# Optimization experiments

Measured on AMD Instinct MI355X. Metric: run time of the kernel, lower is better.

The kernel has to match this reference:

```python
import jax, jax.numpy as jnp
import numpy as np

T, B, L, D = 4, 16, 1024, 256
TAU = 2.0        # LIF membrane time constant
V_TH = 1.0       # spike threshold
ALPHA = 4.0      # sigmoid surrogate slope (spikingjelly default)


@jax.custom_vjp
def spike(x):
    # Heaviside step with sigmoid surrogate gradient
    return (x >= 0.0).astype(x.dtype)

def _spike_fwd(x):
    return spike(x), x

def _spike_bwd(x, g):
    s = jax.nn.sigmoid(ALPHA * x)
    return (g * ALPHA * s * (1.0 - s),)

spike.defvjp(_spike_fwd, _spike_bwd)


def lif_multistep(x):
    """MultiStepLIFNode(tau=2, hard reset to 0, detach_reset=True) over dim 0.
    x: [T, B, 1, D] -> spikes [T, B, 1, D]."""
    def step(v, xt):
        h = v + (xt - v) / TAU                 # neuronal charge
        s = spike(h - V_TH)                    # fire
        v_next = h * (1.0 - jax.lax.stop_gradient(s))  # detached hard reset
        return v_next, s
    _, spikes = jax.lax.scan(step, jnp.zeros_like(x[0]), x)
    return spikes


def setup_inputs() -> dict:
    key = jax.random.key(0)
    kq, kk, kv, km = jax.random.split(key, 4)
    q = jax.random.normal(kq, (T, B, L, D), jnp.float32)
    k = jax.random.normal(kk, (T, B, L, D), jnp.float32)
    v = jax.random.normal(kv, (T, B, L, D), jnp.float32)
    mask = jax.random.randint(km, (T, B, L), 0, 2) > 0  # bool padding mask
    return {"q": q, "k": k, "v": v, "mask": mask}


def reference(q, k, v, mask):
    # mode='s' path of ScaledDotProductAttention
    attn = k * v                                      # [T,B,L,D]
    attn = jnp.where(mask[..., None], 0.0, attn)      # masked_fill(mask, 0)
    kv = jnp.sum(attn, axis=-2, keepdims=True)        # [T,B,1,D]
    kv = lif_multistep(kv)                            # spiking gate over T
    output = q * kv                                   # broadcast over L
    return output, attn
```

## Files before the change

kernel.cpp:

```cpp
#include <hip/hip_runtime.h>

#define T_ 4
#define B_ 16
#define L_ 1024
#define D_ 256
#define TAU_INV 0.5f
#define V_TH 1.0f

constexpr int TB_   = T_ * B_;
constexpr int NELEM = T_ * B_ * L_ * D_;
constexpr int BD_   = B_ * D_;
constexpr int TBD_  = T_ * B_ * D_;

__global__ void init_ws_kernel(float* __restrict__ kv_sum) {
    int i = blockIdx.x * blockDim.x + threadIdx.x;
    if (i < TBD_) kv_sum[i] = 0.0f;
}

#define NCHUNK 16
#define LC 64

__global__ __launch_bounds__(256) void attn_reduce_kernel(
    const float* __restrict__ k, const float* __restrict__ v,
    const int* __restrict__ mask, float* __restrict__ attn_out,
    float* __restrict__ kv_sum)
{
    const int tid   = threadIdx.x;
    const int tb    = blockIdx.x / NCHUNK;
    const int chunk = blockIdx.x % NCHUNK;
    const int d4    = (tid & 63) * 4;
    const int rg    = tid >> 6;

    const int base = tb * (L_ * D_);
    float4 acc = make_float4(0.f, 0.f, 0.f, 0.f);

    #pragma unroll 4
    for (int i = 0; i < LC / 4; ++i) {
        const int l   = chunk * LC + i * 4 + rg;
        const int off = base + l * D_ + d4;
        const float4 kk = *reinterpret_cast<const float4*>(k + off);
        const float4 vv = *reinterpret_cast<const float4*>(v + off);
        const int m = mask[tb * L_ + l];
        float4 a;
        if (m) {
            a = make_float4(0.f, 0.f, 0.f, 0.f);
        } else {
            a.x = kk.x * vv.x; a.y = kk.y * vv.y;
            a.z = kk.z * vv.z; a.w = kk.w * vv.w;
        }
        *reinterpret_cast<float4*>(attn_out + off) = a;
        acc.x += a.x; acc.y += a.y; acc.z += a.z; acc.w += a.w;
    }

    __shared__ float4 red[256];
    red[tid] = acc;
    __syncthreads();
    if (rg == 0) {
        float4 a0 = red[tid];
        float4 a1 = red[tid + 64];
        float4 a2 = red[tid + 128];
        float4 a3 = red[tid + 192];
        float sx = a0.x + a1.x + a2.x + a3.x;
        float sy = a0.y + a1.y + a2.y + a3.y;
        float sz = a0.z + a1.z + a2.z + a3.z;
        float sw = a0.w + a1.w + a2.w + a3.w;
        float* dst = kv_sum + tb * D_ + d4;
        atomicAdd(dst + 0, sx);
        atomicAdd(dst + 1, sy);
        atomicAdd(dst + 2, sz);
        atomicAdd(dst + 3, sw);
    }
}

__global__ void lif_kernel(const float* __restrict__ kv_sum,
                           float* __restrict__ spikes)
{
    const int idx = blockIdx.x * blockDim.x + threadIdx.x;
    if (idx >= BD_) return;
    float vm = 0.0f;
    #pragma unroll
    for (int t = 0; t < T_; ++t) {
        const float x = kv_sum[t * BD_ + idx];
        const float h = vm + (x - vm) * TAU_INV;
        const float s = (h >= V_TH) ? 1.0f : 0.0f;
        spikes[t * BD_ + idx] = s;
        vm = h * (1.0f - s);
    }
}

__global__ __launch_bounds__(256) void qmul_kernel(
    const float* __restrict__ q, const float* __restrict__ spikes,
    float* __restrict__ out)
{
    const int i4 = blockIdx.x * blockDim.x + threadIdx.x;
    if (i4 >= NELEM / 4) return;
    const int d4  = (i4 & 63) * 4;
    const int tbl = i4 >> 6;
    const int tb  = tbl >> 10;
    const float4 qq = reinterpret_cast<const float4*>(q)[i4];
    const float4 ss = *reinterpret_cast<const float4*>(spikes + tb * D_ + d4);
    float4 o;
    o.x = qq.x * ss.x; o.y = qq.y * ss.y;
    o.z = qq.z * ss.z; o.w = qq.w * ss.w;
    reinterpret_cast<float4*>(out)[i4] = o;
}

extern "C" void kernel_launch(void* const* d_in, const int* in_sizes, int n_in,
                              void* d_out, int out_size, void* d_ws, size_t ws_size,
                              hipStream_t stream) {
    const float* q    = (const float*)d_in[0];
    const float* k    = (const float*)d_in[1];
    const float* v    = (const float*)d_in[2];
    const int*   mask = (const int*)d_in[3];

    float* out  = (float*)d_out;
    float* attn = out + NELEM;

    float* kv_sum = (float*)d_ws;
    float* spikes = kv_sum + TBD_;

    init_ws_kernel<<<(TBD_ + 255) / 256, 256, 0, stream>>>(kv_sum);

    attn_reduce_kernel<<<TB_ * NCHUNK, 256, 0, stream>>>(k, v, mask, attn, kv_sum);

    lif_kernel<<<(BD_ + 255) / 256, 256, 0, stream>>>(kv_sum, spikes);

    qmul_kernel<<<NELEM / 4 / 256, 256, 0, stream>>>(q, spikes, out);
}
```

Baseline: 271.9 us.

## Replace atomic reduction with per-chunk partials, add nontemporal loads/stores, more chunks

Removes the workspace init kernel and float atomics by having each block write its chunk partial sum, which the LIF kernel then reduces deterministically. It doubles the number of L-chunks to raise block count, fully unrolls the inner loop, and uses nontemporal loads and stores for the streaming k, v, q and output traffic. The LIF kernel now reads 32 partials per element, which adds a small serial cost. Nontemporal hints may or may not help on this memory-bound streaming workload.

```diff
diff --git a/kernel.cpp b/kernel.cpp
--- a/kernel.cpp
+++ b/kernel.cpp
@@ -12,18 +12,15 @@
 constexpr int BD_   = B_ * D_;
 constexpr int TBD_  = T_ * B_ * D_;
 
-__global__ void init_ws_kernel(float* __restrict__ kv_sum) {
-    int i = blockIdx.x * blockDim.x + threadIdx.x;
-    if (i < TBD_) kv_sum[i] = 0.0f;
-}
+typedef float f4 __attribute__((ext_vector_type(4)));
 
-#define NCHUNK 16
-#define LC 64
+#define NCHUNK 32
+#define LC 32
 
-__global__ __launch_bounds__(256) void attn_reduce_kernel(
+__global__ __launch_bounds__(256) void attn_partial_kernel(
     const float* __restrict__ k, const float* __restrict__ v,
     const int* __restrict__ mask, float* __restrict__ attn_out,
-    float* __restrict__ kv_sum)
+    float* __restrict__ partials)
 {
     const int tid   = threadIdx.x;
     const int tb    = blockIdx.x / NCHUNK;
@@ -32,55 +29,46 @@
     const int rg    = tid >> 6;
 
     const int base = tb * (L_ * D_);
-    float4 acc = make_float4(0.f, 0.f, 0.f, 0.f);
+    f4 acc = (f4)(0.0f);
 
-    #pragma unroll 4
+    #pragma unroll
     for (int i = 0; i < LC / 4; ++i) {
         const int l   = chunk * LC + i * 4 + rg;
         const int off = base + l * D_ + d4;
-        const float4 kk = *reinterpret_cast<const float4*>(k + off);
-        const float4 vv = *reinterpret_cast<const float4*>(v + off);
+        const f4 kk = __builtin_nontemporal_load(reinterpret_cast<const f4*>(k + off));
+        const f4 vv = __builtin_nontemporal_load(reinterpret_cast<const f4*>(v + off));
         const int m = mask[tb * L_ + l];
-        float4 a;
-        if (m) {
-            a = make_float4(0.f, 0.f, 0.f, 0.f);
-        } else {
-            a.x = kk.x * vv.x; a.y = kk.y * vv.y;
-            a.z = kk.z * vv.z; a.w = kk.w * vv.w;
-        }
-        *reinterpret_cast<float4*>(attn_out + off) = a;
-        acc.x += a.x; acc.y += a.y; acc.z += a.z; acc.w += a.w;
+        f4 a = m ? (f4)(0.0f) : (kk * vv);
+        __builtin_nontemporal_store(a, reinterpret_cast<f4*>(attn_out + off));
+        acc += a;
     }
 
-    __shared__ float4 red[256];
+    __shared__ f4 red[256];
     red[tid] = acc;
     __syncthreads();
     if (rg == 0) {
-        float4 a0 = red[tid];
-        float4 a1 = red[tid + 64];
-        float4 a2 = red[tid + 128];
-        float4 a3 = red[tid + 192];
-        float sx = a0.x + a1.x + a2.x + a3.x;
-        float sy = a0.y + a1.y + a2.y + a3.y;
-        float sz = a0.z + a1.z + a2.z + a3.z;
-        float sw = a0.w + a1.w + a2.w + a3.w;
-        float* dst = kv_sum + tb * D_ + d4;
-        atomicAdd(dst + 0, sx);
-        atomicAdd(dst + 1, sy);
-        atomicAdd(dst + 2, sz);
-        atomicAdd(dst + 3, sw);
+        f4 s = red[tid] + red[tid + 64] + red[tid + 128] + red[tid + 192];
+        *reinterpret_cast<f4*>(partials + (tb * NCHUNK + chunk) * D_ + d4) = s;
     }
 }
 
-__global__ void lif_kernel(const float* __restrict__ kv_sum,
+__global__ void lif_kernel(const float* __restrict__ partials,
                            float* __restrict__ spikes)
 {
     const int idx = blockIdx.x * blockDim.x + threadIdx.x;
     if (idx >= BD_) return;
+    const int b = idx >> 8;
+    const int d = idx & 255;
+
     float vm = 0.0f;
     #pragma unroll
     for (int t = 0; t < T_; ++t) {
-        const float x = kv_sum[t * BD_ + idx];
+        const int tb = t * B_ + b;
+        float x = 0.0f;
+        #pragma unroll
+        for (int c = 0; c < NCHUNK; ++c) {
+            x += partials[(tb * NCHUNK + c) * D_ + d];
+        }
         const float h = vm + (x - vm) * TAU_INV;
         const float s = (h >= V_TH) ? 1.0f : 0.0f;
         spikes[t * BD_ + idx] = s;
@@ -97,12 +85,10 @@
     const int d4  = (i4 & 63) * 4;
     const int tbl = i4 >> 6;
     const int tb  = tbl >> 10;
-    const float4 qq = reinterpret_cast<const float4*>(q)[i4];
-    const float4 ss = *reinterpret_cast<const float4*>(spikes + tb * D_ + d4);
-    float4 o;
-    o.x = qq.x * ss.x; o.y = qq.y * ss.y;
-    o.z = qq.z * ss.z; o.w = qq.w * ss.w;
-    reinterpret_cast<float4*>(out)[i4] = o;
+    const f4 qq = __builtin_nontemporal_load(reinterpret_cast<const f4*>(q) + i4);
+    const f4 ss = *reinterpret_cast<const f4*>(spikes + tb * D_ + d4);
+    const f4 o  = qq * ss;
+    __builtin_nontemporal_store(o, reinterpret_cast<f4*>(out) + i4);
 }
 
 extern "C" void kernel_launch(void* const* d_in, const int* in_sizes, int n_in,
@@ -116,14 +102,10 @@
     float* out  = (float*)d_out;
     float* attn = out + NELEM;
 
-    float* kv_sum = (float*)d_ws;
-    float* spikes = kv_sum + TBD_;
+    float* partials = (float*)d_ws;
+    float* spikes   = partials + TB_ * NCHUNK * D_;
 
-    init_ws_kernel<<<(TBD_ + 255) / 256, 256, 0, stream>>>(kv_sum);
-
-    attn_reduce_kernel<<<TB_ * NCHUNK, 256, 0, stream>>>(k, v, mask, attn, kv_sum);
-
-    lif_kernel<<<(BD_ + 255) / 256, 256, 0, stream>>>(kv_sum, spikes);
-
+    attn_partial_kernel<<<TB_ * NCHUNK, 256, 0, stream>>>(k, v, mask, attn, partials);
+    lif_kernel<<<(BD_ + 255) / 256, 256, 0, stream>>>(partials, spikes);
     qmul_kernel<<<NELEM / 4 / 256, 256, 0, stream>>>(q, spikes, out);
 }
```

After: 263.9 us. 1.03x faster.
